# Optimization experiments

Hardware: AMD Instinct MI355X
Metric: run time of the kernel (lower is better)

## Reference

```python
import jax, jax.numpy as jnp
import numpy as np

NHEAD = 12
EPS_Z = 1e-5
EPS_LN = 1e-5


def _zscore_last(t, n):
    # torch .std is unbiased (ddof=1)
    m = t.mean(axis=-1, keepdims=True)
    var = ((t - m) ** 2).sum(axis=-1, keepdims=True) / (n - 1)
    return (t - m) / (jnp.sqrt(var) + EPS_Z)


def _layernorm(x, g, b):
    m = x.mean(axis=-1, keepdims=True)
    v = ((x - m) ** 2).mean(axis=-1, keepdims=True)
    return (x - m) * jax.lax.rsqrt(v + EPS_LN) * g + b


def setup_inputs() -> dict:
    key = jax.random.key(0)
    ks = jax.random.split(key, 20)
    B, T, D, FF, E = 2, 1024, 768, 3072, 4
    p = lambda k, shape: (jax.random.normal(k, shape, jnp.float32) * 0.02)
    return {
        "src": jax.random.normal(ks[0], (B, T, D), jnp.float32),
        "frac": jax.random.uniform(ks[1], (B, T), jnp.float32),
        "Wq": p(ks[2], (D, D)), "bq": jnp.zeros((D,), jnp.float32),
        "Wk": p(ks[3], (D, D)), "bk": jnp.zeros((D,), jnp.float32),
        "Wv": p(ks[4], (D, D)), "bv": jnp.zeros((D,), jnp.float32),
        "Wo": p(ks[5], (D, D)), "bo": jnp.zeros((D,), jnp.float32),
        "gamma": jnp.float32(1.0),
        "ln1_g": jnp.ones((D,), jnp.float32), "ln1_b": jnp.zeros((D,), jnp.float32),
        "ln2_g": jnp.ones((D,), jnp.float32), "ln2_b": jnp.zeros((D,), jnp.float32),
        "Wg": p(ks[6], (E, D)), "bg": jnp.zeros((E,), jnp.float32),
        "W1": p(ks[7], (E, D, FF)), "b1": jnp.zeros((E, FF), jnp.float32),
        "W2": p(ks[8], (E, FF, D)), "b2": jnp.zeros((E, D), jnp.float32),
    }


def reference(src, frac, Wq, bq, Wk, bk, Wv, bv, Wo, bo, gamma,
              ln1_g, ln1_b, ln2_g, ln2_b, Wg, bg, W1, b1, W2, b2):
    B, T, D = src.shape
    H = NHEAD
    hd = D // H
    scale = hd ** -0.5

    # ---- attention (add_frac_bias=False path) ----
    Q = (src @ Wq.T + bq).reshape(B, T, H, hd)
    K = (src @ Wk.T + bk).reshape(B, T, H, hd)
    V = (src @ Wv.T + bv).reshape(B, T, H, hd)
    logits = jnp.einsum('bqhd,bkhd->bhqk', Q, K) * scale
    logits = gamma * _zscore_last(logits, T)
    probs = jax.nn.softmax(logits, axis=-1)
    attn = jnp.einsum('bhqk,bkhd->bqhd', probs, V).reshape(B, T, D)
    attn = attn @ Wo.T + bo

    # ---- residual + norm1 ----
    x = _layernorm(src + attn, ln1_g, ln1_b)

    # ---- MoE top-2 feed-forward ----
    E = Wg.shape[0]
    gate_scores = jax.nn.softmax(x @ Wg.T + bg, axis=-1)          # [B,T,E]
    top2_val, top2_idx = jax.lax.top_k(gate_scores, 2)            # [B,T,2]
    combine = (jax.nn.one_hot(top2_idx, E, dtype=x.dtype)
               * top2_val[..., None]).sum(axis=-2)                # [B,T,E]
    h = jax.nn.relu(jnp.einsum('btd,edf->ebtf', x, W1) + b1[:, None, None, :])
    y = jnp.einsum('ebtf,efd->ebtd', h, W2) + b2[:, None, None, :]
    ff = jnp.einsum('ebtd,bte->btd', y, combine)

    # ---- residual + norm2 ----
    return _layernorm(x + ff, ln2_g, ln2_b)
```

## Files before the change

### kernel.cpp

```cpp
#include <hip/hip_runtime.h>

typedef unsigned short u16;
typedef short bf16x8 __attribute__((ext_vector_type(8)));
typedef float f32x4 __attribute__((ext_vector_type(4)));

#define BB 2
#define TT 1024
#define DD 768
#define HH 12
#define HD 64
#define FFD 3072
#define NE 4
#define NTOK (BB*TT)
#define CROWS 4608
#define SLABZ 3538944L

#define MFMA16(a, b, c) __builtin_amdgcn_mfma_f32_16x16x32_bf16((a), (b), (c), 0, 0, 0)

#define ASYNC16(gsrc, ldst)                                                    \
    __builtin_amdgcn_global_load_lds(                                          \
        (const __attribute__((address_space(1))) void*)(gsrc),                 \
        (__attribute__((address_space(3))) void*)(ldst), 16, 0, 0)

__device__ __forceinline__ float us2f(u16 u) {
    return __uint_as_float(((unsigned int)u) << 16);
}
__device__ __forceinline__ u16 f2us(float f) {
    unsigned int x = __float_as_uint(f);
    x += 0x7fffu + ((x >> 16) & 1u);
    return (u16)(x >> 16);
}

__global__ __launch_bounds__(256) void convert5_kernel(
    const float* __restrict__ src, const float* __restrict__ wq,
    const float* __restrict__ wk, const float* __restrict__ wv,
    const float* __restrict__ wo,
    const float* __restrict__ bq, const float* __restrict__ bk,
    const float* __restrict__ bv,
    u16* __restrict__ src_h, u16* __restrict__ wqkv_h, u16* __restrict__ wo_h,
    float* __restrict__ bqkv)
{
    const int bid = blockIdx.x, tid = threadIdx.x;
    if (bid == 1920) {
        for (int i = tid; i < 3 * DD; i += 256) {
            float v = (i < DD) ? bq[i] : (i < 2 * DD) ? bk[i - DD] : bv[i - 2 * DD];
            bqkv[i] = v;
        }
        return;
    }
    int i = bid * 256 + tid;
    const float* in; u16* out; int off;
    if (i < 196608) { in = src; out = src_h; off = i; }
    else {
        int j = i - 196608; int w = j / 73728; off = j - w * 73728;
        in = (w == 0) ? wq : (w == 1) ? wk : (w == 2) ? wv : wo;
        out = (w < 3) ? wqkv_h + (size_t)w * (DD * DD) : wo_h;
    }
    const float4* p = reinterpret_cast<const float4*>(in) + (size_t)off * 2;
    float4 a = p[0], b = p[1];
    u16 o[8] = {f2us(a.x), f2us(a.y), f2us(a.z), f2us(a.w),
                f2us(b.x), f2us(b.y), f2us(b.z), f2us(b.w)};
    *reinterpret_cast<uint4*>(out + (size_t)off * 8) = *reinterpret_cast<uint4*>(o);
}

__global__ __launch_bounds__(256) void transpose_convert_kernel(
    const float* __restrict__ src, u16* __restrict__ dst,
    int C, int dstStride, long srcZ, long dstZ)
{
    __shared__ float tile[32][33];
    const float* s = src + (size_t)blockIdx.z * srcZ;
    u16* d = dst + (size_t)blockIdx.z * dstZ;
    const int c0 = blockIdx.x * 32, r0 = blockIdx.y * 32;
    const int tid = threadIdx.x;
    {
        const int r = tid >> 3, cs = (tid & 7) * 4;
        float4 v = *reinterpret_cast<const float4*>(&s[(size_t)(r0 + r) * C + c0 + cs]);
        tile[r][cs] = v.x; tile[r][cs + 1] = v.y;
        tile[r][cs + 2] = v.z; tile[r][cs + 3] = v.w;
    }
    __syncthreads();
    {
        const int c = tid >> 3, rs = (tid & 7) * 4;
        u16 o[4] = {f2us(tile[rs][c]), f2us(tile[rs + 1][c]),
                    f2us(tile[rs + 2][c]), f2us(tile[rs + 3][c])};
        *reinterpret_cast<uint2*>(&d[(size_t)(c0 + c) * dstStride + r0 + rs]) =
            *reinterpret_cast<uint2*>(o);
    }
}

__global__ __launch_bounds__(256) void scan_build_kernel(
    const int* __restrict__ epack, int* __restrict__ cnt,
    int* __restrict__ rowtok, int* __restrict__ tok2row)
{
    __shared__ int sc[256][4];
    const int tid = threadIdx.x;
    for (int i = tid; i < CROWS; i += 256) rowtok[i] = 0;
    int ep[8];
    int l0 = 0, l1 = 0, l2 = 0, l3 = 0;
    #pragma unroll
    for (int i = 0; i < 8; i++) {
        const int v = epack[tid * 8 + i];
        ep[i] = v;
        const int a = v & 15, b = (v >> 4) & 15;
        l0 += (a == 0) + (b == 0);
        l1 += (a == 1) + (b == 1);
        l2 += (a == 2) + (b == 2);
        l3 += (a == 3) + (b == 3);
    }
    sc[tid][0] = l0; sc[tid][1] = l1; sc[tid][2] = l2; sc[tid][3] = l3;
    __syncthreads();
    for (int off = 1; off < 256; off <<= 1) {
        int v0 = 0, v1 = 0, v2 = 0, v3 = 0;
        if (tid >= off) {
            v0 = sc[tid - off][0]; v1 = sc[tid - off][1];
            v2 = sc[tid - off][2]; v3 = sc[tid - off][3];
        }
        __syncthreads();
        if (tid >= off) {
            sc[tid][0] += v0; sc[tid][1] += v1;
            sc[tid][2] += v2; sc[tid][3] += v3;
        }
        __syncthreads();
    }
    const int t0 = sc[255][0], t1 = sc[255][1], t2 = sc[255][2], t3 = sc[255][3];
    if (tid == 0) { cnt[0] = t0; cnt[1] = t1; cnt[2] = t2; cnt[3] = t3; }
    const int b1 = (t0 + 127) & ~127;
    const int b2 = b1 + ((t1 + 127) & ~127);
    const int b3 = b2 + ((t2 + 127) & ~127);
    int r0 = sc[tid][0] - l0;
    int r1 = b1 + sc[tid][1] - l1;
    int r2 = b2 + sc[tid][2] - l2;
    int r3 = b3 + sc[tid][3] - l3;
    #pragma unroll
    for (int i = 0; i < 8; i++) {
        const int t = tid * 8 + i;
        const int a = ep[i] & 15, b = (ep[i] >> 4) & 15;
        const int ra = (a == 0) ? r0++ : (a == 1) ? r1++ : (a == 2) ? r2++ : r3++;
        rowtok[ra] = t; tok2row[t * 2] = ra;
        const int rb = (b == 0) ? r0++ : (b == 1) ? r1++ : (b == 2) ? r2++ : r3++;
        rowtok[rb] = t; tok2row[t * 2 + 1] = rb;
    }
}

template<int DB>
__global__ __launch_bounds__(256) void gemm_bt_kernel(
    const u16* __restrict__ A, int lda, long aZ,
    const u16* __restrict__ Bt, int ldb, long bZ,
    int K, int mode, int swz,
    float* __restrict__ outF, u16* __restrict__ outH,
    u16* __restrict__ outH2, u16* __restrict__ outH3,
    int ldc, long cZ,
    const float* __restrict__ biasF, int biasZ,
    const int* __restrict__ rowtok, const int* __restrict__ cntp,
    const float* __restrict__ comb)
{
    __shared__ __align__(16) u16 As[(DB ? 2 : 1) * 128 * 64];
    __shared__ __align__(16) u16 Bs[(DB ? 2 : 1) * 128 * 64];
    const int tid = threadIdx.x;
    int bx, by, z, e = 0, baseE = 0;
    if (swz == 3) {
        const int fid = blockIdx.x;
        const int xcd = fid & 7; int r = fid >> 3;
        const int half = (r >= 96) ? 1 : 0; r -= half * 96;
        bx = r % 6; by = r / 6;
        const int ez = xcd * 2 + half; e = ez >> 2; z = ez & 3;
    } else if (swz == 1) {
        const int fid = blockIdx.x;
        const int xcd = fid & 7; const int r = fid >> 3;
        const int ne = xcd * 12 + (r % 12);
        by = r / 12; bx = ne % 24; e = ne / 24; z = e;
    } else if (swz == 2) {
        const int fid = blockIdx.x;
        const int g = (fid & 7) * 36 + (fid >> 3);
        by = g & 15; bx = g >> 4; z = 0;
    } else {
        bx = blockIdx.x; by = blockIdx.y; z = blockIdx.z;
    }
    if (mode == 2 || mode == 4) {
        const int q0 = (cntp[0] + 127) & ~127;
        const int q1 = (cntp[1] + 127) & ~127;
        const int q2 = (cntp[2] + 127) & ~127;
        baseE = (e > 0 ? q0 : 0) + (e > 1 ? q1 : 0) + (e > 2 ? q2 : 0);
        if (by * 128 >= cntp[e]) return;
    }
    const int m0 = by * 128, n0 = bx * 128;
    const u16* Ab = A + (size_t)z * aZ;
    const u16* Bb = Bt + (size_t)z * bZ;
    if (mode == 4) {
        Ab += (size_t)baseE * lda;
        Bb += (size_t)e * ((size_t)DD * FFD);
    }

    const int wave = tid >> 6, lane = tid & 63;
    const int wm = (wave & 1) * 64, wn = (wave >> 1) * 64;
    const int fm = lane & 15;
    const int g  = lane >> 4;

    const int lr8 = lane >> 3;
    const int cg  = ((lane & 7) ^ lr8) * 8;
    const u16 *aG[4], *bG[4];
    u16 *aL[4], *bL[4];
    #pragma unroll
    for (int i = 0; i < 4; i++) {
        const int rr = wave * 32 + i * 8 + lr8;
        int arow;
        if (mode == 2) arow = rowtok[baseE + m0 + rr];
        else           arow = m0 + rr;
        aG[i] = Ab + (size_t)arow * lda + cg;
        bG[i] = Bb + (size_t)(n0 + rr) * ldb + cg;
        aL[i] = &As[(wave * 32 + i * 8) * 64];
        bL[i] = &Bs[(wave * 32 + i * 8) * 64];
    }

#define STAGE(B, KO) do {                                                      \
        const int _o = (B) * (128 * 64);                                       \
        _Pragma("unroll")                                                      \
        for (int _i = 0; _i < 4; _i++) ASYNC16(aG[_i] + (KO), aL[_i] + _o);    \
        _Pragma("unroll")                                                      \
        for (int _i = 0; _i < 4; _i++) ASYNC16(bG[_i] + (KO), bL[_i] + _o);    \
    } while (0)

    const int c0 = ((g    ) ^ (fm & 7)) * 8;
    const int c1 = ((g + 4) ^ (fm & 7)) * 8;
    const u16* pa[4]; const u16* pb[4];
    #pragma unroll
    for (int i = 0; i < 4; i++) {
        pa[i] = &As[(wm + i * 16 + fm) * 64];
        pb[i] = &Bs[(wn + i * 16 + fm) * 64];
    }

    f32x4 acc[4][4] = {};
    int buf = 0;
    if (DB) STAGE(0, 0);

    for (int k0 = 0; k0 < K; k0 += 64) {
        if (DB) {
            asm volatile("s_waitcnt vmcnt(0)" ::: "memory");
            __builtin_amdgcn_s_barrier();
            __builtin_amdgcn_sched_barrier(0);
            if (k0 + 64 < K) STAGE(buf ^ 1, k0 + 64);
        } else {
            STAGE(0, k0);
            __syncthreads();
        }
        const int bo = DB ? buf * (128 * 64) : 0;
        #pragma unroll
        for (int ks = 0; ks < 2; ks++) {
            const int cc = bo + (ks ? c1 : c0);
            bf16x8 af[4], bf[4];
            #pragma unroll
            for (int i = 0; i < 4; i++)
                af[i] = *reinterpret_cast<const bf16x8*>(pa[i] + cc);
            #pragma unroll
            for (int j = 0; j < 4; j++)
                bf[j] = *reinterpret_cast<const bf16x8*>(pb[j] + cc);
            #pragma unroll
            for (int i = 0; i < 4; i++)
                #pragma unroll
                for (int j = 0; j < 4; j++)
                    acc[i][j] = MFMA16(af[i], bf[j], acc[i][j]);
        }
        if (DB) buf ^= 1;
        else    __syncthreads();
    }
    if (DB) __syncthreads();
#undef STAGE

    const int cn = lane & 15, cr = (lane >> 4) * 4;

    if (mode == 0) {
        const int which = (n0 >= 1536) ? 2 : (n0 >= 768 ? 1 : 0);
        const int nb = n0 - which * 768;
        u16* outP = (which == 0) ? outH : (which == 1) ? outH2 : outH3;
        u16* Cs = As;
        #pragma unroll
        for (int i = 0; i < 4; i++) {
            if (i) __syncthreads();
            #pragma unroll
            for (int j = 0; j < 4; j++) {
                const int n = n0 + wn + j * 16 + cn;
                const float bias = biasF[n];
                #pragma unroll
                for (int r = 0; r < 4; r++) {
                    Cs[((wave & 1) * 16 + cr + r) * 128 + wn + j * 16 + cn] =
                        f2us(acc[i][j][r] + bias);
                }
            }
            __syncthreads();
            if (which < 2) {
                const int lr2 = tid >> 3, c2 = (tid & 7) * 16;
                const int m2 = m0 + (lr2 >> 4) * 64 + i * 16 + (lr2 & 15);
                const int bb2 = m2 >> 10, t2 = m2 & 1023;
                const int hh = (nb + c2) >> 6, d0 = (nb + c2) & 63;
                u16* dst = outP + (((size_t)(bb2 * HH + hh) * TT + t2) << 6) + d0;
                *reinterpret_cast<uint4*>(dst) =
                    *reinterpret_cast<const uint4*>(&Cs[lr2 * 128 + c2]);
                *reinterpret_cast<uint4*>(dst + 8) =
                    *reinterpret_cast<const uint4*>(&Cs[lr2 * 128 + c2 + 8]);
            } else {
                const int nl = tid >> 1, half = tid & 1;
                const int hh = (nb + nl) >> 6, d = (nb + nl) & 63;
                #pragma unroll
                for (int seg = 0; seg < 2; seg++) {
                    u16 o[8];
                    #pragma unroll
                    for (int k = 0; k < 8; k++)
                        o[k] = Cs[(seg * 16 + half * 8 + k) * 128 + nl];
                    const int t0 = m0 + seg * 64 + i * 16 + half * 8;
                    const int bb2 = t0 >> 10, tt2 = t0 & 1023;
                    u16* dst = outP + (((size_t)(bb2 * HH + hh) * HD + d) << 10) + tt2;
                    *reinterpret_cast<uint4*>(dst) = *reinterpret_cast<uint4*>(o);
                }
            }
        }
        return;
    }

    if (mode == 2) {
        u16* Cs = As;
        #pragma unroll
        for (int i = 0; i < 4; i++) {
            if (i) __syncthreads();
            int tokr[4]; float combr[4];
            #pragma unroll
            for (int r = 0; r < 4; r++)
                tokr[r] = rowtok[baseE + m0 + wm + i * 16 + cr + r];
            #pragma unroll
            for (int r = 0; r < 4; r++)
                combr[r] = comb[(size_t)tokr[r] * NE + z];
            #pragma unroll
            for (int j = 0; j < 4; j++) {
                const int n = n0 + wn + j * 16 + cn;
                const float bias = biasF[(size_t)z * biasZ + n];
                #pragma unroll
                for (int r = 0; r < 4; r++) {
                    float y = fmaxf(acc[i][j][r] + bias, 0.f) * combr[r];
                    Cs[((wave & 1) * 16 + cr + r) * 128 + wn + j * 16 + cn] = f2us(y);
                }
            }
            __syncthreads();
            const int lr2 = tid >> 3, c2 = (tid & 7) * 16;
            const int m2 = m0 + (lr2 >> 4) * 64 + i * 16 + (lr2 & 15);
            u16* dst = outH + (size_t)(baseE + m2) * ldc + n0 + c2;
            *reinterpret_cast<uint4*>(dst) =
                *reinterpret_cast<const uint4*>(&Cs[lr2 * 128 + c2]);
            *reinterpret_cast<uint4*>(dst + 8) =
                *reinterpret_cast<const uint4*>(&Cs[lr2 * 128 + c2 + 8]);
        }
        return;
    }

    #pragma unroll
    for (int i = 0; i < 4; i++) {
        #pragma unroll
        for (int j = 0; j < 4; j++) {
            const int n = n0 + wn + j * 16 + cn;
            #pragma unroll
            for (int r = 0; r < 4; r++) {
                const int m = m0 + wm + i * 16 + cr + r;
                float* basep = outF + (size_t)z * cZ;
                basep[(size_t)(baseE + m) * ldc + n] = acc[i][j][r];
            }
        }
    }
}

#define PSTR 1032
__global__ __launch_bounds__(256, 3) void attn_mfma_kernel(
    const u16* __restrict__ Qh, const u16* __restrict__ Kh,
    const u16* __restrict__ VT, const float* __restrict__ gamma_p,
    u16* __restrict__ attn_out)
{
    __shared__ __align__(16) u16 P[16 * PSTR];
    __shared__ __align__(16) float wred[4][16][4];
    __shared__ __align__(16) float dred[16][4];

    const int fid = blockIdx.x;
    const int xcd = fid & 7, rr = fid >> 3;
    const int bh = xcd * 3 + (rr >> 6);
    const int qt = rr & 63;
    const int b = bh / HH, h = bh - b * HH;
    const int tid = threadIdx.x, wave = tid >> 6, lane = tid & 63;
    const int g = lane >> 4, fm = lane & 15;
    const float gamma = gamma_p[0];
    const int m0 = qt * 16;
    const u16* Qp = Qh + (size_t)bh * TT * HD;
    const u16* Kp = Kh + (size_t)bh * TT * HD;
    const u16* Vp = VT + (size_t)bh * HD * TT;

    bf16x8 af[2];
    #pragma unroll
    for (int ks = 0; ks < 2; ks++)
        af[ks] = *reinterpret_cast<const bf16x8*>(
            Qp + (size_t)(m0 + fm) * HD + ks * 32 + g * 8);

    const int n0w = wave * 256;
    f32x4 acc[16] = {};
    #pragma unroll
    for (int nj = 0; nj < 16; nj++) {
        const u16* kp = Kp + (size_t)(n0w + nj * 16 + fm) * HD + g * 8;
        bf16x8 b0 = *reinterpret_cast<const bf16x8*>(kp);
        bf16x8 b1 = *reinterpret_cast<const bf16x8*>(kp + 32);
        acc[nj] = MFMA16(af[0], b0, acc[nj]);
        acc[nj] = MFMA16(af[1], b1, acc[nj]);
    }

    #pragma unroll
    for (int r = 0; r < 4; r++) {
        float s1 = 0.f, s2 = 0.f, mx = -3.4e38f, mn = 3.4e38f;
        #pragma unroll
        for (int nj = 0; nj < 16; nj++) {
            float v = acc[nj][r];
            s1 += v; s2 = fmaf(v, v, s2);
            mx = fmaxf(mx, v); mn = fminf(mn, v);
        }
        #pragma unroll
        for (int msk = 1; msk < 16; msk <<= 1) {
            s1 += __shfl_xor(s1, msk);
            s2 += __shfl_xor(s2, msk);
            mx = fmaxf(mx, __shfl_xor(mx, msk));
            mn = fminf(mn, __shfl_xor(mn, msk));
        }
        if (fm == 0) {
            const int row = g * 4 + r;
            wred[wave][row][0] = s1; wred[wave][row][1] = s2;
            wred[wave][row][2] = mx; wred[wave][row][3] = mn;
        }
    }
    __syncthreads();

    #pragma unroll
    for (int r = 0; r < 4; r++) {
        const int row = g * 4 + r;
        float s1 = 0.f, s2 = 0.f, mx = -3.4e38f, mn = 3.4e38f;
        #pragma unroll
        for (int w = 0; w < 4; w++) {
            float4 t = *reinterpret_cast<const float4*>(&wred[w][row][0]);
            s1 += t.x; s2 += t.y;
            mx = fmaxf(mx, t.z); mn = fminf(mn, t.w);
        }
        float var = (s2 - s1 * s1 * (1.f / TT)) * (1.f / (TT - 1));
        var = fmaxf(var, 0.f);
        const float a = gamma / (sqrtf(var) + 8e-5f);
        const float cm = (a >= 0.f) ? a * mx : a * mn;
        float dp = 0.f;
        #pragma unroll
        for (int nj = 0; nj < 16; nj++) {
            float p = __expf(fmaf(a, acc[nj][r], -cm));
            u16 pb = f2us(p);
            dp += us2f(pb);
            P[row * PSTR + n0w + nj * 16 + fm] = pb;
        }
        #pragma unroll
        for (int msk = 1; msk < 16; msk <<= 1) dp += __shfl_xor(dp, msk);
        if (fm == 0) dred[row][wave] = dp;
    }
    __syncthreads();

    f32x4 oacc = {};
    #pragma unroll 8
    for (int ks = 0; ks < 32; ks++) {
        bf16x8 bv = *reinterpret_cast<const bf16x8*>(
            Vp + (size_t)(wave * 16 + fm) * TT + ks * 32 + g * 8);
        bf16x8 a0 = *reinterpret_cast<const bf16x8*>(&P[(size_t)fm * PSTR + ks * 32 + g * 8]);
        oacc = MFMA16(a0, bv, oacc);
    }

    #pragma unroll
    for (int r = 0; r < 4; r++) {
        const int row = g * 4 + r;
        float4 dv = *reinterpret_cast<const float4*>(&dred[row][0]);
        const float dinv = 1.f / (dv.x + dv.y + dv.z + dv.w);
        const int t = m0 + row;
        attn_out[((size_t)(b * TT + t)) * DD + h * HD + wave * 16 + fm] =
            f2us(oacc[r] * dinv);
    }
}

__global__ __launch_bounds__(256) void ln1_kernel(
    const float* __restrict__ p0, const float* __restrict__ p1,
    const float* __restrict__ p2, const float* __restrict__ p3,
    const float* __restrict__ src, const float* __restrict__ bo,
    const float* __restrict__ g, const float* __restrict__ bta,
    const float* __restrict__ Wg, const float* __restrict__ bg,
    float* __restrict__ outF, u16* __restrict__ outH,
    float* __restrict__ comb, int* __restrict__ epack)
{
    const int row = blockIdx.x, tid = threadIdx.x;
    __shared__ float red[256];
    __shared__ float gred[4][4];
    const size_t base = (size_t)row * DD;
    float v[3];
    #pragma unroll
    for (int i = 0; i < 3; i++) {
        int c = tid + i * 256;
        v[i] = p0[base + c] + p1[base + c] + p2[base + c] + p3[base + c]
             + src[base + c] + bo[c];
    }
    float s = v[0] + v[1] + v[2];
    red[tid] = s; __syncthreads();
    #pragma unroll
    for (int o = 128; o > 0; o >>= 1) { if (tid < o) red[tid] += red[tid + o]; __syncthreads(); }
    const float mean = red[0] * (1.f / 768.f);
    __syncthreads();
    float qv = 0.f;
    #pragma unroll
    for (int i = 0; i < 3; i++) { float d = v[i] - mean; qv += d * d; }
    red[tid] = qv; __syncthreads();
    #pragma unroll
    for (int o = 128; o > 0; o >>= 1) { if (tid < o) red[tid] += red[tid + o]; __syncthreads(); }
    const float var = red[0] * (1.f / 768.f);
    const float rs = rsqrtf(var + 1e-5f);
    float ga0 = 0.f, ga1 = 0.f, ga2 = 0.f, ga3 = 0.f;
    #pragma unroll
    for (int i = 0; i < 3; i++) {
        int c = tid + i * 256;
        float o = (v[i] - mean) * rs * g[c] + bta[c];
        outF[base + c] = o;
        outH[base + c] = f2us(o);
        ga0 = fmaf(o, Wg[c], ga0);
        ga1 = fmaf(o, Wg[DD + c], ga1);
        ga2 = fmaf(o, Wg[2 * DD + c], ga2);
        ga3 = fmaf(o, Wg[3 * DD + c], ga3);
    }
    #pragma unroll
    for (int off = 32; off > 0; off >>= 1) {
        ga0 += __shfl_down(ga0, off, 64);
        ga1 += __shfl_down(ga1, off, 64);
        ga2 += __shfl_down(ga2, off, 64);
        ga3 += __shfl_down(ga3, off, 64);
    }
    const int wave = tid >> 6, lane = tid & 63;
    if (lane == 0) {
        gred[wave][0] = ga0; gred[wave][1] = ga1;
        gred[wave][2] = ga2; gred[wave][3] = ga3;
    }
    __syncthreads();
    if (tid == 0) {
        float gg[NE];
        #pragma unroll
        for (int e = 0; e < NE; e++)
            gg[e] = gred[0][e] + gred[1][e] + gred[2][e] + gred[3][e] + bg[e];
        float m = -1e30f;
        #pragma unroll
        for (int e = 0; e < NE; e++) m = fmaxf(m, gg[e]);
        float ex[NE], ssum = 0.f;
        #pragma unroll
        for (int e = 0; e < NE; e++) { ex[e] = __expf(gg[e] - m); ssum += ex[e]; }
        #pragma unroll
        for (int e = 0; e < NE; e++) ex[e] /= ssum;
        int e1 = 0;
        #pragma unroll
        for (int e = 1; e < NE; e++) if (ex[e] > ex[e1]) e1 = e;
        int e2 = -1;
        #pragma unroll
        for (int e = 0; e < NE; e++) if (e != e1 && (e2 < 0 || ex[e] > ex[e2])) e2 = e;
        float c[NE] = {0.f, 0.f, 0.f, 0.f};
        c[e1] = ex[e1]; c[e2] = ex[e2];
        #pragma unroll
        for (int e = 0; e < NE; e++) comb[(size_t)row * NE + e] = c[e];
        epack[row] = e1 | (e2 << 4);
    }
}

__global__ __launch_bounds__(256) void ln2_kernel(
    const float* __restrict__ x, const float* __restrict__ pslab,
    const int* __restrict__ tok2row,
    const float* __restrict__ comb, const float* __restrict__ b2,
    const float* __restrict__ g, const float* __restrict__ bta,
    float* __restrict__ outF)
{
    const int row = blockIdx.x, tid = threadIdx.x;
    __shared__ float red[256];
    const size_t base = (size_t)row * DD;
    const int r0 = tok2row[row * 2], r1 = tok2row[row * 2 + 1];
    const float* q0 = pslab + (size_t)r0 * DD;
    const float* q1 = pslab + (size_t)r1 * DD;
    const float c0 = comb[row * NE + 0], c1 = comb[row * NE + 1];
    const float c2 = comb[row * NE + 2], c3 = comb[row * NE + 3];
    float v[3];
    #pragma unroll
    for (int i = 0; i < 3; i++) {
        int c = tid + i * 256;
        float t = x[base + c];
        t += q0[c] + q0[SLABZ + c] + q0[2 * SLABZ + c] + q0[3 * SLABZ + c];
        t += q1[c] + q1[SLABZ + c] + q1[2 * SLABZ + c] + q1[3 * SLABZ + c];
        t = fmaf(c0, b2[c], t);
        t = fmaf(c1, b2[DD + c], t);
        t = fmaf(c2, b2[2 * DD + c], t);
        t = fmaf(c3, b2[3 * DD + c], t);
        v[i] = t;
    }
    float s = v[0] + v[1] + v[2];
    red[tid] = s; __syncthreads();
    #pragma unroll
    for (int o = 128; o > 0; o >>= 1) { if (tid < o) red[tid] += red[tid + o]; __syncthreads(); }
    const float mean = red[0] * (1.f / 768.f);
    __syncthreads();
    float qv = 0.f;
    #pragma unroll
    for (int i = 0; i < 3; i++) { float d = v[i] - mean; qv += d * d; }
    red[tid] = qv; __syncthreads();
    #pragma unroll
    for (int o = 128; o > 0; o >>= 1) { if (tid < o) red[tid] += red[tid + o]; __syncthreads(); }
    const float var = red[0] * (1.f / 768.f);
    const float rs = rsqrtf(var + 1e-5f);
    #pragma unroll
    for (int i = 0; i < 3; i++) {
        int c = tid + i * 256;
        outF[base + c] = (v[i] - mean) * rs * g[c] + bta[c];
    }
}

extern "C" void kernel_launch(void* const* d_in, const int* in_sizes, int n_in,
                              void* d_out, int out_size, void* d_ws, size_t ws_size,
                              hipStream_t stream)
{
    const float* src  = (const float*)d_in[0];
    const float* Wq   = (const float*)d_in[2];  const float* bq = (const float*)d_in[3];
    const float* Wk   = (const float*)d_in[4];  const float* bk = (const float*)d_in[5];
    const float* Wv   = (const float*)d_in[6];  const float* bv = (const float*)d_in[7];
    const float* Wo   = (const float*)d_in[8];  const float* bo = (const float*)d_in[9];
    const float* gam  = (const float*)d_in[10];
    const float* ln1g = (const float*)d_in[11]; const float* ln1b = (const float*)d_in[12];
    const float* ln2g = (const float*)d_in[13]; const float* ln2b = (const float*)d_in[14];
    const float* Wg   = (const float*)d_in[15]; const float* bg = (const float*)d_in[16];
    const float* W1   = (const float*)d_in[17]; const float* b1 = (const float*)d_in[18];
    const float* W2   = (const float*)d_in[19]; const float* b2 = (const float*)d_in[20];
    (void)ws_size; (void)in_sizes; (void)n_in; (void)out_size;

    char* ws = (char*)d_ws;
    u16*   W1T  = (u16*)(ws);
    float* wop  = (float*)(ws + 18874368);
    float* pslab= (float*)(ws);
    u16*   W2T  = (u16*)(ws + 56623104);
    u16*   hb   = (u16*)(ws + 75497472);
    float* x    = (float*)(ws + 103809024);
    u16*   xh   = (u16*)(ws + 110100480);
    float* comb = (float*)(ws + 113246208);
    float* bqkv = (float*)(ws + 113278976);
    int*   cnt    = (int*)(ws + 113288192);
    int*   rowtok = (int*)(ws + 113288256);
    int*   epack  = (int*)(ws + 113306688);
    int*   tok2row= (int*)(ws + 113323072);
    char* H = ws + 75497472;
    u16*   Qh     = (u16*)(H);
    u16*   Kh     = (u16*)(H + 3145728);
    u16*   VTh    = (u16*)(H + 6291456);
    u16*   src_h  = (u16*)(H + 9437184);
    u16*   attn_h = (u16*)(H + 12582912);
    u16*   WqkvH  = (u16*)(H + 15728640);
    u16*   WoH    = (u16*)(H + 19267584);
    const long PZ = (long)NTOK * DD;

    convert5_kernel<<<1921, 256, 0, stream>>>(
        src, Wq, Wk, Wv, Wo, bq, bk, bv, src_h, WqkvH, WoH, bqkv);
    transpose_convert_kernel<<<dim3(FFD / 32, DD / 32, NE), 256, 0, stream>>>(
        W1, W1T, FFD, DD, (long)DD * FFD, (long)FFD * DD);
    transpose_convert_kernel<<<dim3(DD / 32, FFD / 32, NE), 256, 0, stream>>>(
        W2, W2T, DD, FFD, (long)FFD * DD, (long)FFD * DD);

    gemm_bt_kernel<1><<<dim3(288, 1, 1), 256, 0, stream>>>(
        src_h, DD, 0, WqkvH, DD, 0, DD, 0, 2,
        nullptr, Qh, Kh, VTh, 0, 0, bqkv, 0, nullptr, nullptr, nullptr);

    attn_mfma_kernel<<<dim3(1536, 1, 1), 256, 0, stream>>>(
        Qh, Kh, VTh, gam, attn_h);

    gemm_bt_kernel<1><<<dim3(DD / 128, NTOK / 128, 4), 256, 0, stream>>>(
        attn_h, DD, 192L, WoH, DD, 192L, 192, 3, 0,
        wop, nullptr, nullptr, nullptr, DD, PZ, nullptr, 0, nullptr, nullptr, nullptr);

    ln1_kernel<<<NTOK, 256, 0, stream>>>(
        wop, wop + PZ, wop + 2 * PZ, wop + 3 * PZ, src, bo,
        ln1g, ln1b, Wg, bg, x, xh, comb, epack);

    scan_build_kernel<<<1, 256, 0, stream>>>(epack, cnt, rowtok, tok2row);

    gemm_bt_kernel<0><<<dim3(1536, 1, 1), 256, 0, stream>>>(
        xh, DD, 0, W1T, DD, (long)FFD * DD, DD, 2, 1,
        nullptr, hb, nullptr, nullptr, FFD, 0, b1, FFD, rowtok, cnt, comb);

    gemm_bt_kernel<0><<<dim3(1536, 1, 1), 256, 0, stream>>>(
        hb, FFD, 768L, W2T, FFD, 768L, 768, 4, 3,
        pslab, nullptr, nullptr, nullptr, DD, SLABZ, nullptr, 0, rowtok, cnt, nullptr);

    ln2_kernel<<<NTOK, 256, 0, stream>>>(
        x, pslab, tok2row, comb, b2, ln2g, ln2b, (float*)d_out);
}
```

Before: 355.5 us.

## Halve split-K for expert down-projection and merge weight transpose launches

The second expert GEMM now splits K=3072 into two chunks of 1536 instead of four of 768, launching half as many blocks. This halves the partial-sum slabs that are written and then read back in the final layernorm kernel. The two W1/W2 transpose-convert launches are also merged into one flat-grid kernel. The trade-off is fewer, longer-running blocks in the down-projection, which may fill the GPU less evenly.

```diff
diff --git a/kernel.cpp b/kernel.cpp
--- a/kernel.cpp
+++ b/kernel.cpp
@@ -63,15 +63,25 @@
     *reinterpret_cast<uint4*>(out + (size_t)off * 8) = *reinterpret_cast<uint4*>(o);
 }
 
-__global__ __launch_bounds__(256) void transpose_convert_kernel(
-    const float* __restrict__ src, u16* __restrict__ dst,
-    int C, int dstStride, long srcZ, long dstZ)
+__global__ __launch_bounds__(256) void transpose_all_kernel(
+    const float* __restrict__ W1, const float* __restrict__ W2,
+    u16* __restrict__ W1T, u16* __restrict__ W2T)
 {
     __shared__ float tile[32][33];
-    const float* s = src + (size_t)blockIdx.z * srcZ;
-    u16* d = dst + (size_t)blockIdx.z * dstZ;
-    const int c0 = blockIdx.x * 32, r0 = blockIdx.y * 32;
-    const int tid = threadIdx.x;
+    const int bid = blockIdx.x, tid = threadIdx.x;
+    const float* s; u16* d; int C, dstStride, c0, r0;
+    if (bid < 9216) {
+        const int e = bid / 2304, rem = bid % 2304;
+        c0 = (rem % 96) * 32; r0 = (rem / 96) * 32;
+        C = FFD; dstStride = DD;
+        s = W1 + (size_t)e * DD * FFD; d = W1T + (size_t)e * FFD * DD;
+    } else {
+        const int b2 = bid - 9216;
+        const int e = b2 / 2304, rem = b2 % 2304;
+        c0 = (rem % 24) * 32; r0 = (rem / 24) * 32;
+        C = DD; dstStride = FFD;
+        s = W2 + (size_t)e * FFD * DD; d = W2T + (size_t)e * FFD * DD;
+    }
     {
         const int r = tid >> 3, cs = (tid & 7) * 4;
         float4 v = *reinterpret_cast<const float4*>(&s[(size_t)(r0 + r) * C + c0 + cs]);
@@ -160,10 +170,9 @@
     int bx, by, z, e = 0, baseE = 0;
     if (swz == 3) {
         const int fid = blockIdx.x;
-        const int xcd = fid & 7; int r = fid >> 3;
-        const int half = (r >= 96) ? 1 : 0; r -= half * 96;
+        const int xcd = fid & 7; const int r = fid >> 3;
         bx = r % 6; by = r / 6;
-        const int ez = xcd * 2 + half; e = ez >> 2; z = ez & 3;
+        e = xcd >> 1; z = xcd & 1;
     } else if (swz == 1) {
         const int fid = blockIdx.x;
         const int xcd = fid & 7; const int r = fid >> 3;
@@ -583,8 +592,8 @@
     for (int i = 0; i < 3; i++) {
         int c = tid + i * 256;
         float t = x[base + c];
-        t += q0[c] + q0[SLABZ + c] + q0[2 * SLABZ + c] + q0[3 * SLABZ + c];
-        t += q1[c] + q1[SLABZ + c] + q1[2 * SLABZ + c] + q1[3 * SLABZ + c];
+        t += q0[c] + q0[SLABZ + c];
+        t += q1[c] + q1[SLABZ + c];
         t = fmaf(c0, b2[c], t);
         t = fmaf(c1, b2[DD + c], t);
         t = fmaf(c2, b2[2 * DD + c], t);
@@ -655,10 +664,7 @@
 
     convert5_kernel<<<1921, 256, 0, stream>>>(
         src, Wq, Wk, Wv, Wo, bq, bk, bv, src_h, WqkvH, WoH, bqkv);
-    transpose_convert_kernel<<<dim3(FFD / 32, DD / 32, NE), 256, 0, stream>>>(
-        W1, W1T, FFD, DD, (long)DD * FFD, (long)FFD * DD);
-    transpose_convert_kernel<<<dim3(DD / 32, FFD / 32, NE), 256, 0, stream>>>(
-        W2, W2T, DD, FFD, (long)FFD * DD, (long)FFD * DD);
+    transpose_all_kernel<<<18432, 256, 0, stream>>>(W1, W2, W1T, W2T);
 
     gemm_bt_kernel<1><<<dim3(288, 1, 1), 256, 0, stream>>>(
         src_h, DD, 0, WqkvH, DD, 0, DD, 0, 2,
@@ -681,8 +687,8 @@
         xh, DD, 0, W1T, DD, (long)FFD * DD, DD, 2, 1,
         nullptr, hb, nullptr, nullptr, FFD, 0, b1, FFD, rowtok, cnt, comb);
 
-    gemm_bt_kernel<0><<<dim3(1536, 1, 1), 256, 0, stream>>>(
-        hb, FFD, 768L, W2T, FFD, 768L, 768, 4, 3,
+    gemm_bt_kernel<0><<<dim3(768, 1, 1), 256, 0, stream>>>(
+        hb, FFD, 1536L, W2T, FFD, 1536L, 1536, 4, 3,
         pslab, nullptr, nullptr, nullptr, DD, SLABZ, nullptr, 0, rowtok, cnt, nullptr);
 
     ln2_kernel<<<NTOK, 256, 0, stream>>>(
```

Result: faster. 340.8 us (-4.1%).
